# Kernel tuning notes

Measured on AMD Instinct MI355X. Metric: run time of the kernel, lower is better.

## Reference

```python
import jax, jax.numpy as jnp
import numpy as np
import math

D_MODEL = 1024
N_HEADS = 16
D_K = D_MODEL // N_HEADS
R_TYPES = 8
B, S = 2, 2048


def setup_inputs() -> dict:
    key = jax.random.key(0)
    ks = jax.random.split(key, 12)
    sc = 0.02
    return {
        "x": jax.random.normal(ks[0], (B, S, D_MODEL), jnp.float32),
        "Wq": jax.random.normal(ks[1], (D_MODEL, D_MODEL), jnp.float32) * sc,
        "bq": jax.random.normal(ks[2], (D_MODEL,), jnp.float32) * sc,
        "Wk": jax.random.normal(ks[3], (D_MODEL, D_MODEL), jnp.float32) * sc,
        "bk": jax.random.normal(ks[4], (D_MODEL,), jnp.float32) * sc,
        "Wv": jax.random.normal(ks[5], (D_MODEL, D_MODEL), jnp.float32) * sc,
        "bv": jax.random.normal(ks[6], (D_MODEL,), jnp.float32) * sc,
        "Wo": jax.random.normal(ks[7], (D_MODEL, D_MODEL), jnp.float32) * sc,
        "bo": jax.random.normal(ks[8], (D_MODEL,), jnp.float32) * sc,
        "resource_bias": jax.random.normal(ks[9], (N_HEADS, R_TYPES, R_TYPES), jnp.float32),
        "resource_mask": jax.random.randint(ks[10], (B, S), 0, R_TYPES, jnp.int32),
        "attention_mask": jnp.ones((B, S), jnp.int32),
    }


def reference(x, resource_mask, attention_mask, Wq, bq, Wk, bk, Wv, bv, Wo, bo, resource_bias):
    # torch nn.Linear: y = x @ W.T + b
    def lin(h, W, b):
        return jnp.einsum("bsd,ed->bse", h, W) + b

    def split_heads(t):  # [B,S,D] -> [B,H,S,d_k]
        return t.reshape(B, S, N_HEADS, D_K).transpose(0, 2, 1, 3)

    Q = split_heads(lin(x, Wq, bq))
    K = split_heads(lin(x, Wk, bk))
    V = split_heads(lin(x, Wv, bv))

    scores = jnp.einsum("bhid,bhjd->bhij", Q, K) / math.sqrt(D_K)  # [B,H,S,S]

    # vectorized resource-bias gather: bias[h, r_i, r_j] added to scores[b,h,i,j]
    r = resource_mask.astype(jnp.int32)  # values guaranteed < R_TYPES
    # resource_bias[:, r[b,i], r[b,j]] -> [B,H,S,S]
    bias = resource_bias[:, r[:, :, None], r[:, None, :]]  # [H,B,S,S]
    scores = scores + bias.transpose(1, 0, 2, 3)

    mask = attention_mask[:, None, None, :]  # [B,1,1,S] broadcast to [B,H,S,S]
    scores = jnp.where(mask == 0, jnp.float32(-1e9), scores)

    attn = jax.nn.softmax(scores, axis=-1)  # dropout is identity in eval
    out = jnp.einsum("bhij,bhjd->bhid", attn, V)
    out = out.transpose(0, 2, 1, 3).reshape(B, S, D_MODEL)
    return jnp.einsum("bsd,ed->bse", out, Wo) + bo
```

## Files before the change

### kernel.cpp

```cpp
#include <hip/hip_runtime.h>
#include <cstdint>

#define D_MODEL 1024
#define NHEADS  16
#define DKH     64
#define DEXT    80
#define SEQ     2048
#define NBATCH  2
#define MROWS   (NBATCH*SEQ)
#define RTYPES  8
#define LOG2E   1.44269504f

typedef __bf16 bf16;
typedef __bf16 bf16x4v __attribute__((ext_vector_type(4)));
typedef __bf16 bf16x8v __attribute__((ext_vector_type(8)));
typedef float  f32x4v  __attribute__((ext_vector_type(4)));
typedef float  f32x16v __attribute__((ext_vector_type(16)));

typedef unsigned int __attribute__((address_space(1))) as1_u32;
typedef unsigned int __attribute__((address_space(3))) as3_u32;

static __device__ __forceinline__ void gload_lds16(const void* g, void* l) {
  __builtin_amdgcn_global_load_lds((const as1_u32*)(uintptr_t)g,
                                   (as3_u32*)(uintptr_t)l, 16, 0, 0);
}

static __device__ __forceinline__ f32x4v mfma16(bf16x8v a, bf16x8v b, f32x4v c) {
  return __builtin_amdgcn_mfma_f32_16x16x32_bf16(a, b, c, 0, 0, 0);
}
static __device__ __forceinline__ f32x16v mfma32(bf16x8v a, bf16x8v b, f32x16v c) {
  return __builtin_amdgcn_mfma_f32_32x32x16_bf16(a, b, c, 0, 0, 0);
}

static __device__ __forceinline__ int xcd_swizzle(int flat, int nwg){
  const int per = nwg >> 3;
  return (flat & 7) * per + (flat >> 3);
}

__global__ void convert_kernel(const float* __restrict__ x,  const float* __restrict__ wq,
                               const float* __restrict__ wk, const float* __restrict__ wv,
                               const float* __restrict__ wo,
                               bf16* __restrict__ xb,  bf16* __restrict__ wqb,
                               bf16* __restrict__ wkb, bf16* __restrict__ wvb,
                               bf16* __restrict__ wob)
{
  int idx = blockIdx.x*256 + threadIdx.x;
  const float* src; bf16* dst; int i;
  if (idx < 524288){ src = x; dst = xb; i = idx; }
  else {
    int off = idx - 524288;
    int r = off >> 17;
    i = off & 131071;
    if (r == 0)      { src = wq; dst = wqb; }
    else if (r == 1) { src = wk; dst = wkb; }
    else if (r == 2) { src = wv; dst = wvb; }
    else             { src = wo; dst = wob; }
  }
  float4 v0 = ((const float4*)src)[2*i];
  float4 v1 = ((const float4*)src)[2*i+1];
  bf16x8v o;
  o[0]=(bf16)v0.x; o[1]=(bf16)v0.y; o[2]=(bf16)v0.z; o[3]=(bf16)v0.w;
  o[4]=(bf16)v1.x; o[5]=(bf16)v1.y; o[6]=(bf16)v1.z; o[7]=(bf16)v1.w;
  ((bf16x8v*)dst)[i] = o;
}

struct GemmOuts { const bf16* W[3]; const float* bia[3]; void* out[3]; };

__global__ __launch_bounds__(256, 3) void gemm_qkv_kernel(
    const bf16* __restrict__ A, GemmOuts args, float qscale,
    const float* __restrict__ rbias, const int* __restrict__ rmask,
    const int* __restrict__ amask, bf16* __restrict__ qext, bf16* __restrict__ kext)
{
  if (blockIdx.x >= 768){
    int i = (blockIdx.x - 768)*256 + threadIdx.x;
    int s  = i & 2047;
    int hh = (i>>11) & 15;
    int bb = (i>>15) & 1;
    int which = i >> 16;
    int t  = rmask[bb*SEQ + s];
    int am = amask[bb*SEQ + s];
    bf16* dst = (which==0 ? qext : kext)
              + ((size_t)(bb*NHEADS + hh)*SEQ + s)*DEXT + 64;
    bf16x8v lo, hi2;
    if (which == 0){
      #pragma unroll
      for (int r=0;r<8;r++) lo[r] = (bf16)(rbias[(hh*RTYPES + t)*RTYPES + r] * LOG2E);
      #pragma unroll
      for (int r=0;r<8;r++) hi2[r] = (bf16)0.f;
      hi2[0] = (bf16)(-1048576.0f);
    } else {
      #pragma unroll
      for (int r=0;r<8;r++) lo[r] = (bf16)((t==r) ? 1.f : 0.f);
      #pragma unroll
      for (int r=0;r<8;r++) hi2[r] = (bf16)0.f;
      hi2[0] = am ? (bf16)0.f : (bf16)1.0f;
    }
    *(bf16x8v*)dst       = lo;
    *(bf16x8v*)(dst + 8) = hi2;
    return;
  }

  const int K  = D_MODEL;
  const int wg = xcd_swizzle(blockIdx.x, 768);
  const int z  = wg >> 8;
  const bf16*  Bw   = args.W[z];
  const float* bias = args.bia[z];
  void* outp        = args.out[z];
  const float scale = (z==0) ? qscale : 1.0f;

  const int n0 = (wg & 7)*128, m0 = ((wg>>3) & 31)*128;
  const int tid = threadIdx.x;
  const int w = tid>>6, lane = tid&63, g = lane>>4, c = lane&15;
  const int wm = w>>1, wn = w&1;

  __shared__ __align__(16) bf16 a_lds[2][128*32];
  __shared__ __align__(16) bf16 b_lds[2][128*32];

  const f32x4v fzero = {0.f,0.f,0.f,0.f};
  f32x4v acc[4][4];
  for (int i=0;i<4;i++) for (int j=0;j<4;j++) acc[i][j] = fzero;

  const int srow = tid>>2, sc8 = tid&3;

  auto STAGE = [&](int k0, int nb){
    gload_lds16(A  + (size_t)(m0+srow)*K     + k0 + sc8*8, &a_lds[nb][(w*64)*8]);
    gload_lds16(Bw + (size_t)(n0+srow)*K     + k0 + sc8*8, &b_lds[nb][(w*64)*8]);
    gload_lds16(A  + (size_t)(m0+64+srow)*K  + k0 + sc8*8, &a_lds[nb][(256 + w*64)*8]);
    gload_lds16(Bw + (size_t)(n0+64+srow)*K  + k0 + sc8*8, &b_lds[nb][(256 + w*64)*8]);
  };

  auto COMPUTE = [&](int nb){
    bf16x8v af[4], bfv[4];
    #pragma unroll
    for (int mt=0;mt<4;mt++)
      af[mt] = *(const bf16x8v*)&a_lds[nb][(wm*64 + mt*16 + c)*32 + g*8];
    #pragma unroll
    for (int nt=0;nt<4;nt++)
      bfv[nt] = *(const bf16x8v*)&b_lds[nb][(wn*64 + nt*16 + c)*32 + g*8];
    #pragma unroll
    for (int mt=0;mt<4;mt++)
      #pragma unroll
      for (int nt=0;nt<4;nt++)
        acc[mt][nt] = mfma16(af[mt], bfv[nt], acc[mt][nt]);
  };

  STAGE(0, 0);
  __syncthreads();
  int cur = 0;
  for (int k0=32; k0<K; k0+=32){
    STAGE(k0, cur^1);
    COMPUTE(cur);
    __syncthreads();
    cur ^= 1;
  }
  COMPUTE(cur);

  #pragma unroll
  for (int mt=0;mt<4;mt++){
    #pragma unroll
    for (int nt=0;nt<4;nt++){
      if (z == 2){
        int m = m0 + wm*64 + mt*16 + g*4;
        int n = n0 + wn*64 + nt*16 + c;
        int bb=m>>11, s=m&2047, hh=n>>6, dk=n&63;
        float bn = bias[n];
        bf16x4v ov;
        #pragma unroll
        for (int r=0;r<4;r++) ov[r] = (bf16)(acc[mt][nt][r] + bn);
        *(bf16x4v*)&((bf16*)outp)[(((size_t)bb*NHEADS+hh)*DKH + dk)*SEQ + s] = ov;
      } else {
        #pragma unroll
        for (int r=0;r<4;r++){
          int m = m0 + wm*64 + mt*16 + g*4 + r;
          int n = n0 + wn*64 + nt*16 + c;
          float v = (acc[mt][nt][r] + bias[n]) * scale;
          int bb=m>>11, s=m&2047, hh=n>>6, dk=n&63;
          ((bf16*)outp)[(((size_t)bb*NHEADS+hh)*SEQ + s)*DEXT + dk] = (bf16)v;
        }
      }
    }
  }
}

__global__ __launch_bounds__(256, 2) void gemm_out_kernel(
    const bf16* __restrict__ A, const bf16* __restrict__ Bw,
    const float* __restrict__ bias, float* __restrict__ outp)
{
  const int K  = D_MODEL;
  const int wg = xcd_swizzle(blockIdx.x, 512);
  const int n0 = (wg & 15)*64, m0 = (wg >> 4)*128;
  const int tid = threadIdx.x;
  const int w = tid>>6, lane = tid&63, g = lane>>4, c = lane&15;
  const int wm = w>>1, wn = w&1;

  __shared__ __align__(16) bf16 a_lds[2][128*32];
  __shared__ __align__(16) bf16 b_lds[2][64*32];

  const f32x4v fzero = {0.f,0.f,0.f,0.f};
  f32x4v acc[4][2];
  for (int i=0;i<4;i++) for (int j=0;j<2;j++) acc[i][j] = fzero;

  const int srow = tid>>2, sc8 = tid&3;

  auto STAGE = [&](int k0, int nb){
    gload_lds16(A  + (size_t)(m0+srow)*K     + k0 + sc8*8, &a_lds[nb][(w*64)*8]);
    gload_lds16(A  + (size_t)(m0+64+srow)*K  + k0 + sc8*8, &a_lds[nb][(256 + w*64)*8]);
    gload_lds16(Bw + (size_t)(n0+srow)*K     + k0 + sc8*8, &b_lds[nb][(w*64)*8]);
  };

  auto COMPUTE = [&](int nb){
    bf16x8v af[4], bfv[2];
    #pragma unroll
    for (int mt=0;mt<4;mt++)
      af[mt] = *(const bf16x8v*)&a_lds[nb][(wm*64 + mt*16 + c)*32 + g*8];
    #pragma unroll
    for (int nt=0;nt<2;nt++)
      bfv[nt] = *(const bf16x8v*)&b_lds[nb][(wn*32 + nt*16 + c)*32 + g*8];
    #pragma unroll
    for (int mt=0;mt<4;mt++)
      #pragma unroll
      for (int nt=0;nt<2;nt++)
        acc[mt][nt] = mfma16(af[mt], bfv[nt], acc[mt][nt]);
  };

  STAGE(0, 0);
  __syncthreads();
  int cur = 0;
  for (int k0=32; k0<K; k0+=32){
    STAGE(k0, cur^1);
    COMPUTE(cur);
    __syncthreads();
    cur ^= 1;
  }
  COMPUTE(cur);

  #pragma unroll
  for (int mt=0;mt<4;mt++){
    #pragma unroll
    for (int nt=0;nt<2;nt++){
      #pragma unroll
      for (int r=0;r<4;r++){
        int m = m0 + wm*64 + mt*16 + g*4 + r;
        int n = n0 + wn*32 + nt*16 + c;
        outp[(size_t)m*D_MODEL + n] = acc[mt][nt][r] + bias[n];
      }
    }
  }
}

__global__ __launch_bounds__(512, 4) void attn10_kernel(
    const bf16* __restrict__ Qg, const bf16* __restrict__ Kg,
    const bf16* __restrict__ Vtg, bf16* __restrict__ Og)
{
  const int wg = xcd_swizzle(blockIdx.x, 512);
  const int q0 = (wg & 15)*128;
  const int h  = (wg >> 4) & 15;
  const int b  = wg >> 8;
  const int tid = threadIdx.x;
  const int w = tid>>6, lane = tid&63;
  const int half = w>>2, wl = w&3;
  const int q5 = lane&31, hi = lane>>5;
  const int bh = b*NHEADS + h;
  const int NTl = 16;

  __shared__ __align__(16) bf16 k_lds[2][2][5120];
  __shared__ __align__(16) bf16 v_lds[2][2][4096];

  const int qrow = q0 + wl*32 + q5;
  const bf16* qptr = Qg + ((size_t)bh*SEQ + qrow)*DEXT;
  bf16x8v qf[5];
  #pragma unroll
  for (int kc=0;kc<5;kc++)
    qf[kc] = *(const bf16x8v*)(qptr + kc*16 + hi*8);

  f32x16v oacc0, oacc1;
  #pragma unroll
  for (int r=0;r<16;r++){ oacc0[r]=0.f; oacc1[r]=0.f; }
  float lrow = 0.f;

  const int sig = (lane & 0x33) | ((lane & 8) >> 1) | ((lane & 4) << 1);
  const bf16* ksrcL = Kg  + ((size_t)bh*SEQ + sig)*DEXT;
  const bf16* vsrcL = Vtg + ((size_t)bh*DKH + lane)*SEQ;
  const int jb0 = half*1024;
  const int lbase = hi*512 + q5*8;

  auto STAGE = [&](int t, int nb){
    const int j0 = jb0 + t*64;
    const size_t joff = (size_t)j0*DEXT;
    gload_lds16(ksrcL + joff + wl*8,       &k_lds[half][nb][wl*512]);
    gload_lds16(ksrcL + joff + (wl+4)*8,   &k_lds[half][nb][(wl+4)*512]);
    if (wl < 2)
      gload_lds16(ksrcL + joff + (8+wl)*8, &k_lds[half][nb][(8+wl)*512]);
    gload_lds16(vsrcL + j0 + wl*8,         &v_lds[half][nb][wl*512]);
    gload_lds16(vsrcL + j0 + (wl+4)*8,     &v_lds[half][nb][(wl+4)*512]);
  };

  auto COMPUTE = [&](int nb){
    const bf16* kb_ = &k_lds[half][nb][0];
    const bf16* vb_ = &v_lds[half][nb][0];

    f32x16v s0, s1;
    #pragma unroll
    for (int r=0;r<16;r++){ s0[r]=0.f; s1[r]=0.f; }
    __builtin_amdgcn_s_setprio(1);
    #pragma unroll
    for (int kc=0;kc<5;kc++){
      bf16x8v kf0 = *(const bf16x8v*)(kb_ + lbase + kc*1024);
      bf16x8v kf1 = *(const bf16x8v*)(kb_ + lbase + kc*1024 + 256);
      s0 = mfma32(kf0, qf[kc], s0);
      s1 = mfma32(kf1, qf[kc], s1);
    }
    __builtin_amdgcn_s_setprio(0);

    #pragma unroll
    for (int r=0;r<16;r++){ s0[r] = exp2f(s0[r]); s1[r] = exp2f(s1[r]); }

    float t0 = 0.f, t1 = 0.f;
    #pragma unroll
    for (int r=0;r<16;r++){ t0 += s0[r]; t1 += s1[r]; }
    float sum = t0 + t1;
    sum += __shfl_xor(sum, 32);
    lrow += sum;

    bf16x8v pa0, pa1, pa2, pa3;
    #pragma unroll
    for (int e=0;e<8;e++){
      pa0[e] = (bf16)s0[e];   pa1[e] = (bf16)s0[e+8];
      pa2[e] = (bf16)s1[e];   pa3[e] = (bf16)s1[e+8];
    }

    __builtin_amdgcn_s_setprio(1);
    #pragma unroll
    for (int m=0;m<4;m++){
      bf16x8v vf0 = *(const bf16x8v*)(vb_ + lbase + m*1024);
      bf16x8v vf1 = *(const bf16x8v*)(vb_ + lbase + m*1024 + 256);
      bf16x8v pm = (m==0)?pa0:(m==1)?pa1:(m==2)?pa2:pa3;
      oacc0 = mfma32(vf0, pm, oacc0);
      oacc1 = mfma32(vf1, pm, oacc1);
    }
    __builtin_amdgcn_s_setprio(0);
  };

  STAGE(0, 0);
  __syncthreads();
  int cur = 0;
  #pragma unroll 1
  for (int t=0; t<NTl; ++t){
    if (t+1 < NTl) STAGE(t+1, cur^1);
    COMPUTE(cur);
    __syncthreads();
    cur ^= 1;
  }

  float* mrg = (float*)&k_lds[0][0][0];
  if (half == 1){
    float* row = mrg + (wl*32 + q5)*68;
    #pragma unroll
    for (int rq=0;rq<4;rq++){
      f32x4v t0v, t1v;
      #pragma unroll
      for (int k=0;k<4;k++){ t0v[k] = oacc0[rq*4+k]; t1v[k] = oacc1[rq*4+k]; }
      *(f32x4v*)(row + 0  + rq*8 + hi*4) = t0v;
      *(f32x4v*)(row + 32 + rq*8 + hi*4) = t1v;
    }
    if (hi == 0) row[64] = lrow;
  }
  __syncthreads();
  if (half == 0){
    const float* row = mrg + (wl*32 + q5)*68;
    const float inv = 1.0f / (lrow + row[64]);
    bf16* orow = &Og[(size_t)(b*SEQ + qrow)*D_MODEL + h*DKH];
    #pragma unroll
    for (int rq=0;rq<4;rq++){
      f32x4v o1a = *(const f32x4v*)(row + 0  + rq*8 + hi*4);
      f32x4v o1b = *(const f32x4v*)(row + 32 + rq*8 + hi*4);
      bf16x4v ov0, ov1;
      #pragma unroll
      for (int k=0;k<4;k++){
        ov0[k] = (bf16)((oacc0[rq*4+k] + o1a[k]) * inv);
        ov1[k] = (bf16)((oacc1[rq*4+k] + o1b[k]) * inv);
      }
      const int d = 8*rq + 4*hi;
      *(bf16x4v*)(orow + d)      = ov0;
      *(bf16x4v*)(orow + 32 + d) = ov1;
    }
  }
}

extern "C" void kernel_launch(void* const* d_in, const int* in_sizes, int n_in,
                              void* d_out, int out_size, void* d_ws, size_t ws_size,
                              hipStream_t stream)
{
  (void)in_sizes; (void)n_in; (void)out_size; (void)ws_size;
  const float* x     = (const float*)d_in[0];
  const float* Wq    = (const float*)d_in[1];
  const float* bq    = (const float*)d_in[2];
  const float* Wk    = (const float*)d_in[3];
  const float* bk    = (const float*)d_in[4];
  const float* Wv    = (const float*)d_in[5];
  const float* bv    = (const float*)d_in[6];
  const float* Wo    = (const float*)d_in[7];
  const float* bo    = (const float*)d_in[8];
  const float* rbias = (const float*)d_in[9];
  const int*   rmask = (const int*)d_in[10];
  const int*   amask = (const int*)d_in[11];
  float* out = (float*)d_out;

  char* ws = (char*)d_ws;
  bf16*  xb    = (bf16*)(ws);
  bf16*  wqb   = (bf16*)(ws + (8u<<20));
  bf16*  wkb   = (bf16*)(ws + (10u<<20));
  bf16*  wvb   = (bf16*)(ws + (12u<<20));
  bf16*  wob   = (bf16*)(ws + (14u<<20));
  bf16*  qb    = (bf16*)(ws + (16u<<20));
  bf16*  kb    = (bf16*)(ws + (27u<<20));
  bf16*  vtb   = (bf16*)(ws + (38u<<20));
  bf16*  aob   = (bf16*)(ws + (46u<<20));

  convert_kernel<<<4096, 256, 0, stream>>>(x,Wq,Wk,Wv,Wo, xb,wqb,wkb,wvb,wob);

  GemmOuts qkv;
  qkv.W[0]=wqb; qkv.W[1]=wkb; qkv.W[2]=wvb;
  qkv.bia[0]=bq; qkv.bia[1]=bk; qkv.bia[2]=bv;
  qkv.out[0]=qb; qkv.out[1]=kb; qkv.out[2]=vtb;
  gemm_qkv_kernel<<<1280, 256, 0, stream>>>(xb, qkv, 0.125f*LOG2E,
                                            rbias, rmask, amask, qb, kb);

  attn10_kernel<<<512, 512, 0, stream>>>(qb, kb, vtb, aob);

  gemm_out_kernel<<<512, 256, 0, stream>>>(aob, wob, bo, out);
}
```

Baseline: 120.5 us.

## Load V fragments directly from global in attention; vectorize Q/K GEMM epilogue stores

The attention kernel no longer stages V through LDS. Each lane now reads its transposed-V MFMA operands straight from global memory (through the cache) inside the compute step. This removes the LDS traffic and LDS footprint for V, but exposes global-load latency that the double buffer no longer hides. Separately, the Q/K projection GEMM swaps the MFMA operand order so each lane holds four consecutive output columns, allowing a vectorized bias load and 4-wide bf16 stores instead of scalar strided stores.

New measurement: 185.2 us. 53.7% more time.

```diff
diff --git a/kernel.cpp b/kernel.cpp
--- a/kernel.cpp
+++ b/kernel.cpp
@@ -137,11 +137,19 @@
     #pragma unroll
     for (int nt=0;nt<4;nt++)
       bfv[nt] = *(const bf16x8v*)&b_lds[nb][(wn*64 + nt*16 + c)*32 + g*8];
-    #pragma unroll
-    for (int mt=0;mt<4;mt++)
-      #pragma unroll
-      for (int nt=0;nt<4;nt++)
-        acc[mt][nt] = mfma16(af[mt], bfv[nt], acc[mt][nt]);
+    if (z == 2){
+      #pragma unroll
+      for (int mt=0;mt<4;mt++)
+        #pragma unroll
+        for (int nt=0;nt<4;nt++)
+          acc[mt][nt] = mfma16(af[mt], bfv[nt], acc[mt][nt]);
+    } else {
+      #pragma unroll
+      for (int mt=0;mt<4;mt++)
+        #pragma unroll
+        for (int nt=0;nt<4;nt++)
+          acc[mt][nt] = mfma16(bfv[nt], af[mt], acc[mt][nt]);
+    }
   };
 
   STAGE(0, 0);
@@ -169,14 +177,14 @@
         for (int r=0;r<4;r++) ov[r] = (bf16)(acc[mt][nt][r] + bn);
         *(bf16x4v*)&((bf16*)outp)[(((size_t)bb*NHEADS+hh)*DKH + dk)*SEQ + s] = ov;
       } else {
+        int m  = m0 + wm*64 + mt*16 + c;
+        int nb_= n0 + wn*64 + nt*16 + g*4;
+        f32x4v b4 = *(const f32x4v*)&bias[nb_];
+        int bb=m>>11, s=m&2047, hh=nb_>>6, dk=nb_&63;
+        bf16x4v ov;
         #pragma unroll
-        for (int r=0;r<4;r++){
-          int m = m0 + wm*64 + mt*16 + g*4 + r;
-          int n = n0 + wn*64 + nt*16 + c;
-          float v = (acc[mt][nt][r] + bias[n]) * scale;
-          int bb=m>>11, s=m&2047, hh=n>>6, dk=n&63;
-          ((bf16*)outp)[(((size_t)bb*NHEADS+hh)*SEQ + s)*DEXT + dk] = (bf16)v;
-        }
+        for (int r=0;r<4;r++) ov[r] = (bf16)((acc[mt][nt][r] + b4[r]) * scale);
+        *(bf16x4v*)&((bf16*)outp)[(((size_t)bb*NHEADS+hh)*SEQ + s)*DEXT + dk] = ov;
       }
     }
   }
@@ -248,7 +256,7 @@
   }
 }
 
-__global__ __launch_bounds__(512, 4) void attn10_kernel(
+__global__ __launch_bounds__(512, 4) void attn13_kernel(
     const bf16* __restrict__ Qg, const bf16* __restrict__ Kg,
     const bf16* __restrict__ Vtg, bf16* __restrict__ Og)
 {
@@ -264,7 +272,6 @@
   const int NTl = 16;
 
   __shared__ __align__(16) bf16 k_lds[2][2][5120];
-  __shared__ __align__(16) bf16 v_lds[2][2][4096];
 
   const int qrow = q0 + wl*32 + q5;
   const bf16* qptr = Qg + ((size_t)bh*SEQ + qrow)*DEXT;
@@ -280,7 +287,8 @@
 
   const int sig = (lane & 0x33) | ((lane & 8) >> 1) | ((lane & 4) << 1);
   const bf16* ksrcL = Kg  + ((size_t)bh*SEQ + sig)*DEXT;
-  const bf16* vsrcL = Vtg + ((size_t)bh*DKH + lane)*SEQ;
+  const bf16* vbase0 = Vtg + ((size_t)bh*DKH + q5)*SEQ;
+  const bf16* vbase1 = Vtg + ((size_t)bh*DKH + 32 + q5)*SEQ;
   const int jb0 = half*1024;
   const int lbase = hi*512 + q5*8;
 
@@ -291,13 +299,17 @@
     gload_lds16(ksrcL + joff + (wl+4)*8,   &k_lds[half][nb][(wl+4)*512]);
     if (wl < 2)
       gload_lds16(ksrcL + joff + (8+wl)*8, &k_lds[half][nb][(8+wl)*512]);
-    gload_lds16(vsrcL + j0 + wl*8,         &v_lds[half][nb][wl*512]);
-    gload_lds16(vsrcL + j0 + (wl+4)*8,     &v_lds[half][nb][(wl+4)*512]);
-  };
-
-  auto COMPUTE = [&](int nb){
+  };
+
+  auto COMPUTE = [&](int nb, int j0){
     const bf16* kb_ = &k_lds[half][nb][0];
-    const bf16* vb_ = &v_lds[half][nb][0];
+
+    bf16x8v vp0[4], vp1[4];
+    #pragma unroll
+    for (int m=0;m<4;m++){
+      vp0[m] = *(const bf16x8v*)(vbase0 + j0 + m*16 + hi*8);
+      vp1[m] = *(const bf16x8v*)(vbase1 + j0 + m*16 + hi*8);
+    }
 
     f32x16v s0, s1;
     #pragma unroll
@@ -332,11 +344,9 @@
     __builtin_amdgcn_s_setprio(1);
     #pragma unroll
     for (int m=0;m<4;m++){
-      bf16x8v vf0 = *(const bf16x8v*)(vb_ + lbase + m*1024);
-      bf16x8v vf1 = *(const bf16x8v*)(vb_ + lbase + m*1024 + 256);
       bf16x8v pm = (m==0)?pa0:(m==1)?pa1:(m==2)?pa2:pa3;
-      oacc0 = mfma32(vf0, pm, oacc0);
-      oacc1 = mfma32(vf1, pm, oacc1);
+      oacc0 = mfma32(vp0[m], pm, oacc0);
+      oacc1 = mfma32(vp1[m], pm, oacc1);
     }
     __builtin_amdgcn_s_setprio(0);
   };
@@ -347,7 +357,7 @@
   #pragma unroll 1
   for (int t=0; t<NTl; ++t){
     if (t+1 < NTl) STAGE(t+1, cur^1);
-    COMPUTE(cur);
+    COMPUTE(cur, jb0 + t*64);
     __syncthreads();
     cur ^= 1;
   }
@@ -426,7 +436,7 @@
   gemm_qkv_kernel<<<1280, 256, 0, stream>>>(xb, qkv, 0.125f*LOG2E,
                                             rbias, rmask, amask, qb, kb);
 
-  attn10_kernel<<<512, 512, 0, stream>>>(qb, kb, vtb, aob);
+  attn13_kernel<<<512, 512, 0, stream>>>(qb, kb, vtb, aob);
 
   gemm_out_kernel<<<512, 256, 0, stream>>>(aob, wob, bo, out);
 }
```
